# Performance work log

Measured on AMD Instinct MI355X. Metric: run time of the kernel, lower is better.

Reference implementation:

```python
import jax, jax.numpy as jnp
import numpy as np

B, C2, H, W = 4, 1024, 64, 64  # features have 2*input_dim channels
CH = C2 // 2                   # 512 = input_dim
HID = CH // 4                  # 128 = hidden_channels


def setup_inputs() -> dict:
    key = jax.random.key(0)
    ks = jax.random.split(key, 6)
    left = jax.random.normal(ks[0], (B, C2, H, W), dtype=jnp.float32)
    right = jax.random.normal(ks[1], (B, C2, H, W), dtype=jnp.float32)
    # 1x1 conv params (weight [out,in], bias [out]) for query/reference projections
    Wq = jax.random.normal(ks[2], (HID, CH), dtype=jnp.float32) * 0.02
    bq = jax.random.normal(ks[3], (HID,), dtype=jnp.float32) * 0.02
    Wk = jax.random.normal(ks[4], (HID, CH), dtype=jnp.float32) * 0.02
    bk = jax.random.normal(ks[5], (HID,), dtype=jnp.float32) * 0.02
    return {"left_features": left, "right_features": right, "Wq": Wq, "bq": bq, "Wk": Wk, "bk": bk}


def _co_attention(qf, rf, Wq, bq, Wk, bk):
    # 1x1 convs == per-pixel channel matmuls
    Q = jnp.einsum('bchw,oc->bohw', qf, Wq) + bq[None, :, None, None]   # [B,HID,H,W]
    K = jnp.einsum('bchw,oc->bohw', rf, Wk) + bk[None, :, None, None]   # [B,HID,H,W]
    b, c, h, w = Q.shape
    Kf = K.reshape(b, c, h * w)                                          # [B,HID,P]
    V = rf.reshape(rf.shape[0], rf.shape[1], h * w)                      # [B,CH,P]
    # attention_map: einsum('bcij,bckl->bijkl') then flatten (kl) == contract channels
    attn = jnp.einsum('bcij,bcp->bijp', Q, Kf)                           # [B,H,W,P]
    attn = jax.nn.softmax(attn, axis=3)
    return jnp.einsum('bijp,bcp->bcij', attn, V)                         # [B,CH,H,W]


def _homo(qf, rf):
    weights = jax.nn.softmax(qf - rf, axis=1)  # softmax over channels
    return rf * weights


def _get_both_differences(q, r, Wq, bq, Wk, bk):
    c = q.shape[1] // 2
    q_orig, q_trans = q[:, :c], q[:, c:]
    r_orig = r[:, :c]
    cross = _co_attention(q_orig, r_orig, Wq, bq, Wk, bk)
    reduce = _homo(q_orig, q_trans)
    return jnp.concatenate([q_orig, cross + reduce], axis=1)


def reference(left_features, right_features, Wq, bq, Wk, bk):
    left_out = _get_both_differences(left_features, right_features, Wq, bq, Wk, bk)
    right_out = _get_both_differences(right_features, left_features, Wq, bq, Wk, bk)
    return (left_out, right_out)
```

## Files before the change

kernel.cpp:

```cpp
#include <hip/hip_runtime.h>
#include <hip/hip_bf16.h>

#define NB 4
#define LOG2E 1.4426950408889634f

typedef unsigned short u16;
typedef __attribute__((ext_vector_type(8))) short bf16x8;
typedef __attribute__((ext_vector_type(4))) float f32x4;

static __device__ __forceinline__ float bf2f(u16 u) {
    union { float f; unsigned v; } x; x.v = ((unsigned)u) << 16; return x.f;
}
static __device__ __forceinline__ u16 f2bf(float f) {
    unsigned v = __builtin_bit_cast(unsigned, f);
    return (u16)((v + 0x7FFFu + ((v >> 16) & 1u)) >> 16);
}
static __device__ __forceinline__ void gload_lds16(const u16* g, u16* l) {
    __builtin_amdgcn_global_load_lds(
        (const __attribute__((address_space(1))) unsigned*)(const void*)g,
        (__attribute__((address_space(3))) unsigned*)(void*)l, 16, 0, 0);
}

__global__ void k_wcvt(const float* __restrict__ Wq, const float* __restrict__ Wk,
                       u16* __restrict__ Wbq, u16* __restrict__ Wbk) {
    int i = blockIdx.x * 1024 + threadIdx.x;
    Wbq[i] = f2bf(Wq[i]);
    Wbk[i] = f2bf(Wk[i]);
}

__global__ __launch_bounds__(256) void k_cvtf(
        const float* __restrict__ L, const float* __restrict__ R,
        u16* __restrict__ Lb, u16* __restrict__ Rb,
        u16* __restrict__ web, float* __restrict__ sumsH, float* __restrict__ out) {
    __shared__ float pred[4][1024];
    int idx = blockIdx.x;
    int sb = idx & 7, pseg = (idx >> 3) & 3, cpart = idx >> 5;
    int side = sb & 1, b = sb >> 1;
    int osb = side * 4 + b;
    const float* src = (side ? R : L) + (size_t)b * 1024 * 4096;
    u16* lbbase = (side ? Rb : Lb) + (size_t)b * 512 * 4096;
    int tid = threadIdx.x, wv = tid >> 6, lane = tid & 63;
    int p0 = pseg * 1024;
    int cA = cpart * 8 + wv * 2;
#pragma unroll
    for (int s = 0; s < 4; s++) {
        int p = p0 + s * 256 + lane * 4;
        float4 sm = {0.f, 0.f, 0.f, 0.f};
#pragma unroll
        for (int cc = 0; cc < 2; cc++) {
            int c = cA + cc;
            float4 a = *reinterpret_cast<const float4*>(src + (size_t)c * 4096 + p);
            float4 t = *reinterpret_cast<const float4*>(src + (size_t)(512 + c) * 4096 + p);
            ushort4 ub;
            ub.x = f2bf(a.x); ub.y = f2bf(a.y); ub.z = f2bf(a.z); ub.w = f2bf(a.w);
            *reinterpret_cast<ushort4*>(lbbase + (size_t)c * 4096 + p) = ub;
            *reinterpret_cast<float4*>(out + ((size_t)osb * 1024 + c) * 4096 + p) = a;
            float4 e;
            e.x = exp2f((a.x - t.x) * LOG2E);
            e.y = exp2f((a.y - t.y) * LOG2E);
            e.z = exp2f((a.z - t.z) * LOG2E);
            e.w = exp2f((a.w - t.w) * LOG2E);
            sm.x += e.x; sm.y += e.y; sm.z += e.z; sm.w += e.w;
            ushort4 wb_;
            wb_.x = f2bf(t.x * e.x); wb_.y = f2bf(t.y * e.y);
            wb_.z = f2bf(t.z * e.z); wb_.w = f2bf(t.w * e.w);
            *reinterpret_cast<ushort4*>(web + ((size_t)osb * 512 + c) * 4096 + p) = wb_;
        }
        *reinterpret_cast<float4*>(&pred[wv][s * 256 + lane * 4]) = sm;
    }
    __syncthreads();
    {
        float4 t0 = *reinterpret_cast<const float4*>(&pred[0][tid * 4]);
        float4 t1 = *reinterpret_cast<const float4*>(&pred[1][tid * 4]);
        float4 t2 = *reinterpret_cast<const float4*>(&pred[2][tid * 4]);
        float4 t3 = *reinterpret_cast<const float4*>(&pred[3][tid * 4]);
        float4 tot;
        tot.x = (t0.x + t1.x) + (t2.x + t3.x);
        tot.y = (t0.y + t1.y) + (t2.y + t3.y);
        tot.z = (t0.z + t1.z) + (t2.z + t3.z);
        tot.w = (t0.w + t1.w) + (t2.w + t3.w);
        *reinterpret_cast<float4*>(
            sumsH + ((size_t)cpart * 8 + osb) * 4096 + p0 + tid * 4) = tot;
    }
}

__global__ __launch_bounds__(256) void k_hsum(const float* __restrict__ sumsH,
                                              float* __restrict__ hinv) {
    int i = blockIdx.x * 256 + threadIdx.x;
    float4 tot = {0.f, 0.f, 0.f, 0.f};
    for (int cp = 0; cp < 64; cp++) {
        float4 v = *reinterpret_cast<const float4*>(sumsH + (size_t)cp * 8 * 4096 + (size_t)i * 4);
        tot.x += v.x; tot.y += v.y; tot.z += v.z; tot.w += v.w;
    }
    float4 r = {1.0f / tot.x, 1.0f / tot.y, 1.0f / tot.z, 1.0f / tot.w};
    *reinterpret_cast<float4*>(hinv + (size_t)i * 4) = r;
}

__global__ void k_cvt(const float* __restrict__ L, const float* __restrict__ R,
                      u16* __restrict__ Lb, u16* __restrict__ Rb, float* __restrict__ out) {
    int i = blockIdx.x * 256 + threadIdx.x;
    int pq = i & 1023;
    int c = (i >> 10) & 511;
    int b = (i >> 19) & 3;
    int side = i >> 21;
    const float* src = (side ? R : L) + ((long)(b * 1024 + c) << 12) + (pq << 2);
    float4 v = *reinterpret_cast<const float4*>(src);
    ushort4 u;
    u.x = f2bf(v.x); u.y = f2bf(v.y); u.z = f2bf(v.z); u.w = f2bf(v.w);
    *reinterpret_cast<ushort4*>((side ? Rb : Lb) + ((long)(b * 512 + c) << 12) + (pq << 2)) = u;
    *reinterpret_cast<float4*>(out + ((long)(side * 4 + b) * 1024 + c) * 4096 + (pq << 2)) = v;
}

__global__ __launch_bounds__(256) void k_proj(
        const u16* __restrict__ Lb, const u16* __restrict__ Rb,
        const u16* __restrict__ Wbq, const u16* __restrict__ Wbk,
        const float* __restrict__ bq, const float* __restrict__ bk,
        u16* __restrict__ QL, u16* __restrict__ KL,
        u16* __restrict__ QR, u16* __restrict__ KR) {
    __shared__ u16 XT[2][64 * 40];
    int pj = blockIdx.x & 15, pt = blockIdx.x >> 4;
    int ty = pj >> 2, b = pj & 3;
    const u16* src; const u16* Wb; const float* bias; u16* dst;
    if (ty == 0)      { src = Lb; Wb = Wbq; bias = bq; dst = QL; }
    else if (ty == 1) { src = Rb; Wb = Wbk; bias = bk; dst = KL; }
    else if (ty == 2) { src = Rb; Wb = Wbq; bias = bq; dst = QR; }
    else              { src = Lb; Wb = Wbk; bias = bk; dst = KR; }
    const u16* X = src + (long)b * 512 * 4096 + pt * 64;
    int tid = threadIdx.x;
    int wv = __builtin_amdgcn_readfirstlane(tid >> 6);
    int lane = tid & 63, g = lane >> 4, li = lane & 15;

    f32x4 acc[8];
#pragma unroll
    for (int ob = 0; ob < 8; ob++)
#pragma unroll
        for (int r = 0; r < 4; r++) acc[ob][r] = bias[ob * 16 + g * 4 + r];

    int c_r = tid >> 3, j = tid & 7;
    bf16x8 gx = *reinterpret_cast<const bf16x8*>(X + (long)c_r * 4096 + j * 8);
#pragma unroll
    for (int k = 0; k < 8; k++) XT[0][(j * 8 + k) * 40 + c_r] = (u16)gx[k];
    __syncthreads();

    for (int cc = 0; cc < 16; cc++) {
        int buf = cc & 1;
        bf16x8 gn;
        if (cc < 15)
            gn = *reinterpret_cast<const bf16x8*>(X + (long)(cc * 32 + 32 + c_r) * 4096 + j * 8);
        bf16x8 xb = *reinterpret_cast<const bf16x8*>(&XT[buf][(wv * 16 + li) * 40 + g * 8]);
#pragma unroll
        for (int ob = 0; ob < 8; ob++) {
            bf16x8 aw = *reinterpret_cast<const bf16x8*>(Wb + (long)(ob * 16 + li) * 512 + cc * 32 + g * 8);
            acc[ob] = __builtin_amdgcn_mfma_f32_16x16x32_bf16(aw, xb, acc[ob], 0, 0, 0);
        }
        if (cc < 15) {
#pragma unroll
            for (int k = 0; k < 8; k++) XT[buf ^ 1][(j * 8 + k) * 40 + c_r] = (u16)gn[k];
        }
        __syncthreads();
    }
    u16* d = dst + ((long)b * 4096 + pt * 64 + wv * 16 + li) * 128;
#pragma unroll
    for (int ob = 0; ob < 8; ob++) {
        uint2 w;
        w.x = (unsigned)f2bf(acc[ob][0]) | ((unsigned)f2bf(acc[ob][1]) << 16);
        w.y = (unsigned)f2bf(acc[ob][2]) | ((unsigned)f2bf(acc[ob][3]) << 16);
        *reinterpret_cast<uint2*>(d + ob * 16 + g * 4) = w;
    }
}

__global__ __launch_bounds__(512, 8) void k_qk(
        const u16* __restrict__ QL, const u16* __restrict__ KL,
        const u16* __restrict__ QR, const u16* __restrict__ KR,
        u16* __restrict__ P, float* __restrict__ sums,
        int bd0, int nbdLog2) {
    __shared__ u16 Kl[2][8192];
    __shared__ u16 Ps[4096];
    int blk = (int)blockIdx.x;
    int bdl = blk & ((1 << nbdLog2) - 1);
    int rest = blk >> nbdLog2;
    int ph0 = rest & 3;
    int qtile = rest >> 2;
    int bd = bd0 + bdl, dir = bd & 1, b = bd >> 1;
    const u16* Qt = (dir ? QR : QL) + (size_t)b * 4096 * 128;
    const u16* Kt = (dir ? KR : KL) + (size_t)b * 4096 * 128;
    u16* Pbd = P + ((size_t)bdl << 24);
    int q0 = qtile * 64;
    int tid = threadIdx.x;
    int wv = __builtin_amdgcn_readfirstlane(tid >> 6);
    int lane = tid & 63, g = lane >> 4, li = lane & 15;
    int qt = wv >> 1, phw = wv & 1;

#define STAGE_K(BUF, PT)                                                                   \
    {                                                                                      \
        _Pragma("unroll") for (int r0 = 0; r0 < 2; r0++) {                                 \
            int o = r0 * 8192 + tid * 16;                                                  \
            int row = o >> 8, w = o & 255;                                                 \
            int sw = (w ^ ((row & 7) << 4)) >> 1;                                          \
            gload_lds16(Kt + (((size_t)((PT) * 64 + row)) << 7) + sw,                      \
                        &Kl[BUF][r0 * 4096 + wv * 512]);                                   \
        }                                                                                  \
    }

    bf16x8 qf[4];
#pragma unroll
    for (int hc = 0; hc < 4; hc++)
        qf[hc] = *reinterpret_cast<const bf16x8*>(
            Qt + (size_t)(q0 + qt * 16 + li) * 128 + hc * 32 + g * 8);
    float psum = 0.f;
    STAGE_K(0, ph0 * 16)

    for (int tt = 0; tt < 16; tt++) {
        int pt = ph0 * 16 + tt;
        if (tt == 0) asm volatile("s_waitcnt vmcnt(0) lgkmcnt(0)\n\ts_barrier" ::: "memory");
        else         asm volatile("s_waitcnt vmcnt(1) lgkmcnt(0)\n\ts_barrier" ::: "memory");
        if (tt < 15) STAGE_K((tt + 1) & 1, pt + 1)
        int buf = tt & 1;
        f32x4 sv[2];
        sv[0] = (f32x4){0.f, 0.f, 0.f, 0.f};
        sv[1] = (f32x4){0.f, 0.f, 0.f, 0.f};
        __builtin_amdgcn_s_setprio(1);
#pragma unroll
        for (int ps = 0; ps < 2; ps++) {
            int row = phw * 32 + ps * 16 + li;
            unsigned rb = (unsigned)row * 256;
            unsigned sz = (unsigned)((row & 7) << 4);
#pragma unroll
            for (int hc = 0; hc < 4; hc++) {
                bf16x8 kf = *reinterpret_cast<const bf16x8*>(
                    (char*)Kl[buf] + rb + (((unsigned)(hc * 64 + g * 16)) ^ sz));
                sv[ps] = __builtin_amdgcn_mfma_f32_16x16x32_bf16(kf, qf[hc], sv[ps], 0, 0, 0);
            }
        }
        __builtin_amdgcn_s_setprio(0);
        int qrow = qt * 16 + li;
        unsigned qsz = (unsigned)((qrow & 7) << 4);
#pragma unroll
        for (int ps = 0; ps < 2; ps++) {
            float e0 = exp2f(sv[ps][0] * LOG2E);
            float e1 = exp2f(sv[ps][1] * LOG2E);
            float e2 = exp2f(sv[ps][2] * LOG2E);
            float e3 = exp2f(sv[ps][3] * LOG2E);
            psum += (e0 + e1) + (e2 + e3);
            uint2 pk;
            pk.x = (unsigned)f2bf(e0) | ((unsigned)f2bf(e1) << 16);
            pk.y = (unsigned)f2bf(e2) | ((unsigned)f2bf(e3) << 16);
            unsigned off = (unsigned)qrow * 128 +
                           (((unsigned)(phw * 64 + ps * 32 + g * 8)) ^ qsz);
            *reinterpret_cast<uint2*>((char*)Ps + off) = pk;
        }
        asm volatile("s_waitcnt lgkmcnt(0)\n\ts_barrier" ::: "memory");
        {
            uint4 d = *reinterpret_cast<const uint4*>((char*)Ps + tid * 16);
            *reinterpret_cast<uint4*>(
                Pbd + ((size_t)(qtile * 64 + pt) << 12) + tid * 8) = d;
        }
    }
    __syncthreads();
    float (*sred)[2][16] = (float(*)[2][16])(void*)Ps;
    psum += __shfl_xor(psum, 16);
    psum += __shfl_xor(psum, 32);
    if (lane < 16) sred[qt][phw][li] = psum;
    __syncthreads();
    if (phw == 0 && lane < 16) {
        float s = sred[qt][0][li] + sred[qt][1][li];
        sums[((size_t)ph0 * 8 + bd) * 4096 + q0 + qt * 16 + li] = s;
    }
#undef STAGE_K
}

template<int FUSEH>
__global__ __launch_bounds__(256, 2) void k_pvC(
        const u16* __restrict__ Lb, const u16* __restrict__ Rb,
        const u16* __restrict__ P, const float* __restrict__ sums,
        const u16* __restrict__ web, const float* __restrict__ hinvArr,
        float* __restrict__ out, int bd0, int bdMask, int bdShift) {
    __shared__ u16 Tl[2][2][8192];
    int bdl, idx;
    if (bdMask == 3) {
        int xcd = (int)blockIdx.x & 7;
        bdl = xcd >> 1;
        idx = (((int)blockIdx.x >> 3) << 1) | (xcd & 1);
    } else {
        bdl = (int)blockIdx.x & bdMask;
        idx = (int)blockIdx.x >> bdShift;
    }
    int mtile = idx & 3;
    int ntile = idx >> 2;
    int bd = bd0 + bdl, dir = bd & 1, b = bd >> 1;
    int osb = dir * 4 + b;
    const u16* V = (dir ? Lb : Rb) + (size_t)b * 512 * 4096;
    const u16* Pbd = P + ((size_t)bdl << 24);
    int q0 = ntile * 128, c0 = mtile * 128, qt0 = ntile * 2;
    int tid = threadIdx.x;
    int wv = __builtin_amdgcn_readfirstlane(tid >> 6);
    int lane = tid & 63, g = lane >> 4, li = lane & 15;
    int wr = wv >> 1, wc = wv & 1;

#define STAGE_PV(BUF, T)                                                                   \
    {                                                                                      \
        _Pragma("unroll") for (int r0 = 0; r0 < 4; r0++) {                                 \
            int o = r0 * 4096 + tid * 16;                                                  \
            int row = o >> 7, w = o & 127;                                                 \
            int sw = (w ^ ((row & 7) << 4)) >> 1;                                          \
            gload_lds16(V + (((size_t)(c0 + row)) << 12) + (T) * 64 + sw,                  \
                        &Tl[BUF][0][r0 * 2048 + wv * 512]);                                \
            gload_lds16(Pbd + (((size_t)((qt0 + (r0 >> 1)) * 64 + (T))) << 12) +           \
                            (r0 & 1) * 2048 + tid * 8,                                     \
                        &Tl[BUF][1][r0 * 2048 + wv * 512]);                                \
        }                                                                                  \
    }

    f32x4 acc[4][4];
#pragma unroll
    for (int i = 0; i < 4; i++)
#pragma unroll
        for (int j = 0; j < 4; j++) acc[i][j] = (f32x4){0.f, 0.f, 0.f, 0.f};

    STAGE_PV(0, 0)

    for (int t = 0; t < 64; t++) {
        asm volatile("s_waitcnt vmcnt(0) lgkmcnt(0)\n\ts_barrier" ::: "memory");
        if (t < 63) STAGE_PV((t + 1) & 1, t + 1)
        int buf = t & 1;
        bf16x8 af[4][2], bf[4][2];
#pragma unroll
        for (int mi = 0; mi < 4; mi++) {
            int row = wr * 64 + mi * 16 + li;
            unsigned rb = (unsigned)row * 128, sz = (unsigned)((row & 7) << 4);
#pragma unroll
            for (int kk = 0; kk < 2; kk++)
                af[mi][kk] = *reinterpret_cast<const bf16x8*>(
                    (char*)Tl[buf][0] + rb + (((unsigned)(kk * 64 + g * 16)) ^ sz));
        }
#pragma unroll
        for (int ni = 0; ni < 4; ni++) {
            int row = wc * 64 + ni * 16 + li;
            unsigned rb = (unsigned)row * 128, sz = (unsigned)((row & 7) << 4);
#pragma unroll
            for (int kk = 0; kk < 2; kk++)
                bf[ni][kk] = *reinterpret_cast<const bf16x8*>(
                    (char*)Tl[buf][1] + rb + (((unsigned)(kk * 64 + g * 16)) ^ sz));
        }
        __builtin_amdgcn_s_setprio(1);
#pragma unroll
        for (int kk = 0; kk < 2; kk++)
#pragma unroll
            for (int mi = 0; mi < 4; mi++)
#pragma unroll
                for (int ni = 0; ni < 4; ni++)
                    acc[mi][ni] = __builtin_amdgcn_mfma_f32_16x16x32_bf16(
                        af[mi][kk], bf[ni][kk], acc[mi][ni], 0, 0, 0);
        __builtin_amdgcn_s_setprio(0);
    }

    float* obase = out + ((size_t)osb * 1024 + 512) * 4096;
    const u16* wb = web + (size_t)osb * 512 * 4096;
#pragma unroll
    for (int ni = 0; ni < 4; ni++) {
        int q = q0 + wc * 64 + ni * 16 + li;
        float s = sums[(size_t)bd * 4096 + q] +
                  sums[((size_t)8 + bd) * 4096 + q] +
                  sums[((size_t)16 + bd) * 4096 + q] +
                  sums[((size_t)24 + bd) * 4096 + q];
        float linv = 1.0f / s;
        float hinv = 0.f;
        if (FUSEH) hinv = hinvArr[(size_t)osb * 4096 + q];
#pragma unroll
        for (int mi = 0; mi < 4; mi++) {
            int c = c0 + wr * 64 + mi * 16 + g * 4;
#pragma unroll
            for (int r = 0; r < 4; r++) {
                float v = acc[mi][ni][r] * linv;
                if (FUSEH) v += bf2f(wb[(size_t)(c + r) * 4096 + q]) * hinv;
                obase[(size_t)(c + r) * 4096 + q] = v;
            }
        }
    }
#undef STAGE_PV
}

__global__ __launch_bounds__(256) void k_homo(const float* __restrict__ L,
                                              const float* __restrict__ R,
                                              float* __restrict__ out) {
    __shared__ float4 red[16][16];
    int sb = blockIdx.x & 7, pblk = blockIdx.x >> 3;
    int side = sb & 1, b = sb >> 1;
    const float* src = (side ? R : L) + (long)b * 1024 * 4096;
    float* o = out + (long)(side * 4 + b) * 1024 * 4096;
    int p4 = threadIdx.x & 15, cg = threadIdx.x >> 4;
    int p = pblk * 64 + p4 * 4;
    const float* qo = src + p;
    const float* qt = src + (long)512 * 4096 + p;
    float4 sm = {0.f, 0.f, 0.f, 0.f};
    for (int c = cg * 32; c < cg * 32 + 32; c++) {
        float4 a = *reinterpret_cast<const float4*>(qo + (long)c * 4096);
        float4 t = *reinterpret_cast<const float4*>(qt + (long)c * 4096);
        sm.x += exp2f((a.x - t.x) * LOG2E);
        sm.y += exp2f((a.y - t.y) * LOG2E);
        sm.z += exp2f((a.z - t.z) * LOG2E);
        sm.w += exp2f((a.w - t.w) * LOG2E);
    }
    red[cg][p4] = sm;
    __syncthreads();
    float4 tot = {0.f, 0.f, 0.f, 0.f};
#pragma unroll
    for (int gR = 0; gR < 16; gR++) {
        float4 v = red[gR][p4];
        tot.x += v.x; tot.y += v.y; tot.z += v.z; tot.w += v.w;
    }
    float4 rinv = {1.0f / tot.x, 1.0f / tot.y, 1.0f / tot.z, 1.0f / tot.w};
    for (int c = cg * 32; c < cg * 32 + 32; c++) {
        float4 a = *reinterpret_cast<const float4*>(qo + (long)c * 4096);
        float4 t = *reinterpret_cast<const float4*>(qt + (long)c * 4096);
        float4* op = reinterpret_cast<float4*>(o + (long)(512 + c) * 4096 + p);
        float4 cur = *op;
        cur.x += t.x * exp2f((a.x - t.x) * LOG2E) * rinv.x;
        cur.y += t.y * exp2f((a.y - t.y) * LOG2E) * rinv.y;
        cur.z += t.z * exp2f((a.z - t.z) * LOG2E) * rinv.z;
        cur.w += t.w * exp2f((a.w - t.w) * LOG2E) * rinv.w;
        *op = cur;
    }
}

extern "C" void kernel_launch(void* const* d_in, const int* in_sizes, int n_in,
                              void* d_out, int out_size, void* d_ws, size_t ws_size,
                              hipStream_t stream) {
    const float* L  = (const float*)d_in[0];
    const float* R  = (const float*)d_in[1];
    const float* Wq = (const float*)d_in[2];
    const float* bq = (const float*)d_in[3];
    const float* Wk = (const float*)d_in[4];
    const float* bk = (const float*)d_in[5];
    float* out = (float*)d_out;
    char* ws = (char*)d_ws;

    size_t off = 0;
    u16* Wbq = (u16*)(ws + off); off += (size_t)128 * 512 * 2;
    u16* Wbk = (u16*)(ws + off); off += (size_t)128 * 512 * 2;
    u16* QL = (u16*)(ws + off); off += (size_t)NB * 4096 * 128 * 2;
    u16* KL = (u16*)(ws + off); off += (size_t)NB * 4096 * 128 * 2;
    u16* QR = (u16*)(ws + off); off += (size_t)NB * 4096 * 128 * 2;
    u16* KR = (u16*)(ws + off); off += (size_t)NB * 4096 * 128 * 2;
    u16* Lb = (u16*)(ws + off); off += (size_t)NB * 512 * 4096 * 2;
    u16* Rb = (u16*)(ws + off); off += (size_t)NB * 512 * 4096 * 2;
    float* sums = (float*)(ws + off); off += (size_t)4 * 8 * 4096 * 4;
    float* hinv = (float*)(ws + off); off += (size_t)8 * 4096 * 4;
    size_t off_nofuse = off;
    float* sumsH = (float*)(ws + off); off += (size_t)64 * 8 * 4096 * 4;
    u16* web = (u16*)(ws + off); off += (size_t)8 * 512 * 4096 * 2;
    off = (off + 255) & ~(size_t)255;
    size_t pchunk4 = (size_t)4 * 4096 * 4096 * 2;

    k_wcvt <<<64, 1024, 0, stream>>>(Wq, Wk, Wbq, Wbk);

    if (ws_size >= off + pchunk4) {
        u16* Pb = (u16*)(ws + off);
        k_cvtf <<<2048, 256, 0, stream>>>(L, R, Lb, Rb, web, sumsH, out);
        k_hsum <<<32,   256, 0, stream>>>(sumsH, hinv);
        k_proj <<<1024, 256, 0, stream>>>(Lb, Rb, Wbq, Wbk, bq, bk, QL, KL, QR, KR);
        for (int c = 0; c < 2; c++) {
            k_qk     <<<1024, 512, 0, stream>>>(QL, KL, QR, KR, Pb, sums, c * 4, 2);
            k_pvC<1> <<<512,  256, 0, stream>>>(Lb, Rb, Pb, sums, web, hinv, out, c * 4, 3, 2);
        }
    } else {
        size_t poff = (off_nofuse + 255) & ~(size_t)255;
        u16* Pb = (u16*)(ws + poff);
        k_cvt  <<<16384, 256, 0, stream>>>(L, R, Lb, Rb, out);
        k_proj <<<1024,  256, 0, stream>>>(Lb, Rb, Wbq, Wbk, bq, bk, QL, KL, QR, KR);
        for (int c = 0; c < 8; c++) {
            k_qk     <<<256, 512, 0, stream>>>(QL, KL, QR, KR, Pb, sums, c, 0);
            k_pvC<0> <<<128, 256, 0, stream>>>(Lb, Rb, Pb, sums, web, hinv, out, c, 0, 0);
        }
        k_homo <<<512, 256, 0, stream>>>(L, R, out);
    }
}
```

Baseline: 381.6 us.

## Add 256x256-tile PV kernel and single-pass full-P path when workspace allows

After: 430.4 us. +12.8%, slower.

```diff
diff --git a/kernel.cpp b/kernel.cpp
--- a/kernel.cpp
+++ b/kernel.cpp
@@ -270,6 +270,121 @@
 }
 
 template<int FUSEH>
+__global__ __launch_bounds__(512, 1) void k_pv256(
+        const u16* __restrict__ Lb, const u16* __restrict__ Rb,
+        const u16* __restrict__ P, const float* __restrict__ sums,
+        const u16* __restrict__ web, const float* __restrict__ hinvArr,
+        float* __restrict__ out) {
+    __shared__ u16 Va[2][16384];
+    __shared__ u16 Pa[2][16384];
+    int bd = (int)blockIdx.x & 7;
+    int idx = (int)blockIdx.x >> 3;
+    int mt = idx & 1, nt = idx >> 1;
+    int dir = bd & 1, b = bd >> 1, osb = dir * 4 + b;
+    const u16* V = (dir ? Lb : Rb) + (size_t)b * 512 * 4096;
+    const u16* Pbd = P + ((size_t)bd << 24);
+    int c0 = mt * 256, q0 = nt * 256;
+    int tid = threadIdx.x;
+    int wv = __builtin_amdgcn_readfirstlane(tid >> 6);
+    int lane = tid & 63, g = lane >> 4, li = lane & 15;
+    int wr = wv >> 2, wc = wv & 3;
+
+    int vsw = (((tid & 7) * 16) ^ (((tid >> 3) & 7) << 4)) >> 1;
+    const u16* vbase = V + (size_t)(c0 + (tid >> 3)) * 4096 + vsw;
+    const u16* pbase = Pbd + (size_t)tid * 8;
+    int ntq = nt * 256;
+
+#define STG_V(OTH, H, K1)                                                              \
+    gload_lds16(vbase + (size_t)((H) * 128) * 4096 + (K1) * 64,                        \
+                &Va[OTH][(H) * 8192 + wv * 512]);                                      \
+    gload_lds16(vbase + (size_t)((H) * 128 + 64) * 4096 + (K1) * 64,                   \
+                &Va[OTH][(H) * 8192 + 4096 + wv * 512]);
+#define STG_P(OTH, H, K1)                                                              \
+    gload_lds16(pbase + (size_t)(ntq + (H) * 128 + (K1)) * 4096,                       \
+                &Pa[OTH][(H) * 8192 + wv * 512]);                                      \
+    gload_lds16(pbase + (size_t)(ntq + (H) * 128 + 64 + (K1)) * 4096,                  \
+                &Pa[OTH][(H) * 8192 + 4096 + wv * 512]);
+
+#define RD_AF(MB, KK)                                                                  \
+    _Pragma("unroll") for (int m_ = 0; m_ < 4; m_++) {                                 \
+        int row = wr * 128 + ((MB) + m_) * 16 + li;                                    \
+        af[m_] = *reinterpret_cast<const bf16x8*>((char*)Va[bufv] + row * 128 +        \
+                 (((unsigned)((KK) * 64 + g * 16)) ^ ((row & 7) << 4)));               \
+    }
+#define RD_BF(KK)                                                                      \
+    _Pragma("unroll") for (int n_ = 0; n_ < 4; n_++) {                                 \
+        int row = wc * 64 + n_ * 16 + li;                                              \
+        bf[n_] = *reinterpret_cast<const bf16x8*>((char*)Pa[bufv] + row * 128 +        \
+                 (((unsigned)((KK) * 64 + g * 16)) ^ ((row & 7) << 4)));               \
+    }
+#define MM(MB)                                                                         \
+    __builtin_amdgcn_s_setprio(1);                                                     \
+    _Pragma("unroll") for (int m_ = 0; m_ < 4; m_++)                                   \
+        _Pragma("unroll") for (int n_ = 0; n_ < 4; n_++)                               \
+            acc[(MB) + m_][n_] = __builtin_amdgcn_mfma_f32_16x16x32_bf16(              \
+                af[m_], bf[n_], acc[(MB) + m_][n_], 0, 0, 0);                          \
+    __builtin_amdgcn_s_setprio(0);
+
+    f32x4 acc[8][4];
+#pragma unroll
+    for (int i = 0; i < 8; i++)
+#pragma unroll
+        for (int j = 0; j < 4; j++) acc[i][j] = (f32x4){0.f, 0.f, 0.f, 0.f};
+
+    STG_V(0, 0, 0) STG_V(0, 1, 0) STG_P(0, 0, 0) STG_P(0, 1, 0)
+
+    for (int k = 0; k < 64; ++k) {
+        int bufv = k & 1, oth = bufv ^ 1;
+        bf16x8 af[4], bf[4];
+        if (k < 63) {
+            STG_V(oth, 0, k + 1)
+            asm volatile("s_waitcnt vmcnt(2)" ::: "memory");
+        } else {
+            asm volatile("s_waitcnt vmcnt(0)" ::: "memory");
+        }
+        asm volatile("s_barrier" ::: "memory");
+        RD_AF(0, 0) RD_BF(0) MM(0)
+        if (k < 63) { STG_P(oth, 0, k + 1) }
+        RD_AF(4, 0) MM(4)
+        if (k < 63) { STG_V(oth, 1, k + 1) }
+        RD_AF(0, 1) RD_BF(1) MM(0)
+        if (k < 63) { STG_P(oth, 1, k + 1) }
+        RD_AF(4, 1) MM(4)
+        asm volatile("s_waitcnt lgkmcnt(0)" ::: "memory");
+        asm volatile("s_barrier" ::: "memory");
+    }
+
+    float* obase = out + ((size_t)osb * 1024 + 512) * 4096;
+    const u16* wb = web + (size_t)osb * 512 * 4096;
+#pragma unroll
+    for (int ni = 0; ni < 4; ni++) {
+        int q = q0 + wc * 64 + ni * 16 + li;
+        float s = sums[(size_t)bd * 4096 + q] +
+                  sums[((size_t)8 + bd) * 4096 + q] +
+                  sums[((size_t)16 + bd) * 4096 + q] +
+                  sums[((size_t)24 + bd) * 4096 + q];
+        float linv = 1.0f / s;
+        float hinv = 0.f;
+        if (FUSEH) hinv = hinvArr[(size_t)osb * 4096 + q];
+#pragma unroll
+        for (int mi = 0; mi < 8; mi++) {
+            int c = c0 + wr * 128 + mi * 16 + g * 4;
+#pragma unroll
+            for (int r = 0; r < 4; r++) {
+                float v = acc[mi][ni][r] * linv;
+                if (FUSEH) v += bf2f(wb[(size_t)(c + r) * 4096 + q]) * hinv;
+                obase[(size_t)(c + r) * 4096 + q] = v;
+            }
+        }
+    }
+#undef STG_V
+#undef STG_P
+#undef RD_AF
+#undef RD_BF
+#undef MM
+}
+
+template<int FUSEH>
 __global__ __launch_bounds__(256, 2) void k_pvC(
         const u16* __restrict__ Lb, const u16* __restrict__ Rb,
         const u16* __restrict__ P, const float* __restrict__ sums,
@@ -451,10 +566,18 @@
     u16* web = (u16*)(ws + off); off += (size_t)8 * 512 * 4096 * 2;
     off = (off + 255) & ~(size_t)255;
     size_t pchunk4 = (size_t)4 * 4096 * 4096 * 2;
+    size_t pfull   = (size_t)8 * 4096 * 4096 * 2;
 
     k_wcvt <<<64, 1024, 0, stream>>>(Wq, Wk, Wbq, Wbk);
 
-    if (ws_size >= off + pchunk4) {
+    if (ws_size >= off + pfull) {
+        u16* Pb = (u16*)(ws + off);
+        k_cvtf     <<<2048, 256, 0, stream>>>(L, R, Lb, Rb, web, sumsH, out);
+        k_hsum     <<<32,   256, 0, stream>>>(sumsH, hinv);
+        k_proj     <<<1024, 256, 0, stream>>>(Lb, Rb, Wbq, Wbk, bq, bk, QL, KL, QR, KR);
+        k_qk       <<<2048, 512, 0, stream>>>(QL, KL, QR, KR, Pb, sums, 0, 3);
+        k_pv256<1> <<<256,  512, 0, stream>>>(Lb, Rb, Pb, sums, web, hinv, out);
+    } else if (ws_size >= off + pchunk4) {
         u16* Pb = (u16*)(ws + off);
         k_cvtf <<<2048, 256, 0, stream>>>(L, R, Lb, Rb, web, sumsH, out);
         k_hsum <<<32,   256, 0, stream>>>(sumsH, hinv);
```

## Process all eight batch-directions in one QK and new larger-tile PV kernel

Applied to the files above, without the earlier changes.

Result: slower. 407.6 us (+6.8%).

```diff
diff --git a/kernel.cpp b/kernel.cpp
--- a/kernel.cpp
+++ b/kernel.cpp
@@ -270,6 +270,134 @@
 }
 
 template<int FUSEH>
+__global__ __launch_bounds__(256, 2) void k_pvD(
+        const u16* __restrict__ Lb, const u16* __restrict__ Rb,
+        const u16* __restrict__ P, const float* __restrict__ sums,
+        const u16* __restrict__ web, const float* __restrict__ hinvArr,
+        float* __restrict__ out) {
+    __shared__ u16 Va[2][8192];
+    __shared__ u16 Pl[2][4096];
+    int bd = (int)blockIdx.x & 7;
+    int idx = (int)blockIdx.x >> 3;
+    int mtile = idx & 1, ntile = idx >> 1;
+    int dir = bd & 1, b = bd >> 1, osb = dir * 4 + b;
+    const u16* V = (dir ? Lb : Rb) + (size_t)b * 512 * 4096;
+    const u16* Pbd = P + ((size_t)bd << 24);
+    int q0 = ntile * 128, c0 = mtile * 256;
+    int tid = threadIdx.x;
+    int wv = __builtin_amdgcn_readfirstlane(tid >> 6);
+    int lane = tid & 63, g = lane >> 4, li = lane & 15;
+    int wr = wv >> 1, wc = wv & 1;
+
+    const u16 *vsrc0, *vsrc1, *vsrc2, *vsrc3;
+    {
+        int o, row, wd;
+        o = tid * 16;          row = o >> 6; wd = (o & 63) ^ (((row >> 1) & 3) << 4);
+        vsrc0 = V + (size_t)(c0 + row) * 4096 + (wd >> 1);
+        o = 4096 + tid * 16;   row = o >> 6; wd = (o & 63) ^ (((row >> 1) & 3) << 4);
+        vsrc1 = V + (size_t)(c0 + row) * 4096 + (wd >> 1);
+        o = 8192 + tid * 16;   row = o >> 6; wd = (o & 63) ^ (((row >> 1) & 3) << 4);
+        vsrc2 = V + (size_t)(c0 + row) * 4096 + (wd >> 1);
+        o = 12288 + tid * 16;  row = o >> 6; wd = (o & 63) ^ (((row >> 1) & 3) << 4);
+        vsrc3 = V + (size_t)(c0 + row) * 4096 + (wd >> 1);
+    }
+    const u16 *pb0, *pb1;
+    int pOff0a, pOff0b, pOff1a, pOff1b;
+    {
+        int o, row, wd, q, qr;
+        o = tid * 16; row = o >> 6; wd = (o & 63) ^ (((row >> 1) & 3) << 4);
+        q = q0 + row; qr = q & 63;
+        pb0 = Pbd + (((size_t)((q >> 6) * 64)) << 12) + qr * 64;
+        pOff0a = ((0  + wd) ^ ((qr & 7) << 4)) >> 1;
+        pOff0b = ((64 + wd) ^ ((qr & 7) << 4)) >> 1;
+        o = 4096 + tid * 16; row = o >> 6; wd = (o & 63) ^ (((row >> 1) & 3) << 4);
+        q = q0 + row; qr = q & 63;
+        pb1 = Pbd + (((size_t)((q >> 6) * 64)) << 12) + qr * 64;
+        pOff1a = ((0  + wd) ^ ((qr & 7) << 4)) >> 1;
+        pOff1b = ((64 + wd) ^ ((qr & 7) << 4)) >> 1;
+    }
+
+#define STAGE_D(BUF, T)                                                                    \
+    {                                                                                      \
+        int pt_ = (T) >> 1, pc_ = (T) & 1;                                                 \
+        gload_lds16(vsrc0 + (T) * 32, &Va[BUF][wv * 512]);                                 \
+        gload_lds16(vsrc1 + (T) * 32, &Va[BUF][2048 + wv * 512]);                          \
+        gload_lds16(vsrc2 + (T) * 32, &Va[BUF][4096 + wv * 512]);                          \
+        gload_lds16(vsrc3 + (T) * 32, &Va[BUF][6144 + wv * 512]);                          \
+        gload_lds16(pb0 + ((size_t)pt_ << 12) + (pc_ ? pOff0b : pOff0a),                   \
+                    &Pl[BUF][wv * 512]);                                                   \
+        gload_lds16(pb1 + ((size_t)pt_ << 12) + (pc_ ? pOff1b : pOff1a),                   \
+                    &Pl[BUF][2048 + wv * 512]);                                            \
+    }
+
+    unsigned aoff[8], boff[4];
+#pragma unroll
+    for (int mi = 0; mi < 8; mi++) {
+        int row = wr * 128 + mi * 16 + li;
+        aoff[mi] = (unsigned)row * 64 + (((unsigned)(g * 16)) ^ (((row >> 1) & 3) << 4));
+    }
+#pragma unroll
+    for (int ni = 0; ni < 4; ni++) {
+        int row = wc * 64 + ni * 16 + li;
+        boff[ni] = (unsigned)row * 64 + (((unsigned)(g * 16)) ^ (((row >> 1) & 3) << 4));
+    }
+
+    f32x4 acc[8][4];
+#pragma unroll
+    for (int i = 0; i < 8; i++)
+#pragma unroll
+        for (int j = 0; j < 4; j++) acc[i][j] = (f32x4){0.f, 0.f, 0.f, 0.f};
+
+    STAGE_D(0, 0)
+
+    for (int t = 0; t < 128; t++) {
+        asm volatile("s_waitcnt vmcnt(0) lgkmcnt(0)\n\ts_barrier" ::: "memory");
+        if (t < 127) STAGE_D((t + 1) & 1, t + 1)
+        int buf = t & 1;
+        bf16x8 af[8], bf[4];
+#pragma unroll
+        for (int mi = 0; mi < 8; mi++)
+            af[mi] = *reinterpret_cast<const bf16x8*>((char*)Va[buf] + aoff[mi]);
+#pragma unroll
+        for (int ni = 0; ni < 4; ni++)
+            bf[ni] = *reinterpret_cast<const bf16x8*>((char*)Pl[buf] + boff[ni]);
+        __builtin_amdgcn_s_setprio(1);
+#pragma unroll
+        for (int mi = 0; mi < 8; mi++)
+#pragma unroll
+            for (int ni = 0; ni < 4; ni++)
+                acc[mi][ni] = __builtin_amdgcn_mfma_f32_16x16x32_bf16(
+                    af[mi], bf[ni], acc[mi][ni], 0, 0, 0);
+        __builtin_amdgcn_s_setprio(0);
+    }
+
+    float* obase = out + ((size_t)osb * 1024 + 512) * 4096;
+    const u16* wb = web + (size_t)osb * 512 * 4096;
+#pragma unroll
+    for (int ni = 0; ni < 4; ni++) {
+        int q = q0 + wc * 64 + ni * 16 + li;
+        float s = sums[(size_t)bd * 4096 + q] +
+                  sums[((size_t)8 + bd) * 4096 + q] +
+                  sums[((size_t)16 + bd) * 4096 + q] +
+                  sums[((size_t)24 + bd) * 4096 + q];
+        float linv = 1.0f / s;
+        float hinv = 0.f;
+        if (FUSEH) hinv = hinvArr[(size_t)osb * 4096 + q];
+#pragma unroll
+        for (int mi = 0; mi < 8; mi++) {
+            int c = c0 + wr * 128 + mi * 16 + g * 4;
+#pragma unroll
+            for (int r = 0; r < 4; r++) {
+                float v = acc[mi][ni][r] * linv;
+                if (FUSEH) v += bf2f(wb[(size_t)(c + r) * 4096 + q]) * hinv;
+                obase[(size_t)(c + r) * 4096 + q] = v;
+            }
+        }
+    }
+#undef STAGE_D
+}
+
+template<int FUSEH>
 __global__ __launch_bounds__(256, 2) void k_pvC(
         const u16* __restrict__ Lb, const u16* __restrict__ Rb,
         const u16* __restrict__ P, const float* __restrict__ sums,
@@ -451,10 +579,18 @@
     u16* web = (u16*)(ws + off); off += (size_t)8 * 512 * 4096 * 2;
     off = (off + 255) & ~(size_t)255;
     size_t pchunk4 = (size_t)4 * 4096 * 4096 * 2;
+    size_t pfull   = (size_t)8 * 4096 * 4096 * 2;
 
     k_wcvt <<<64, 1024, 0, stream>>>(Wq, Wk, Wbq, Wbk);
 
-    if (ws_size >= off + pchunk4) {
+    if (ws_size >= off + pfull) {
+        u16* Pb = (u16*)(ws + off);
+        k_cvtf   <<<2048, 256, 0, stream>>>(L, R, Lb, Rb, web, sumsH, out);
+        k_hsum   <<<32,   256, 0, stream>>>(sumsH, hinv);
+        k_proj   <<<1024, 256, 0, stream>>>(Lb, Rb, Wbq, Wbk, bq, bk, QL, KL, QR, KR);
+        k_qk     <<<2048, 512, 0, stream>>>(QL, KL, QR, KR, Pb, sums, 0, 3);
+        k_pvD<1> <<<512,  256, 0, stream>>>(Lb, Rb, Pb, sums, web, hinv, out);
+    } else if (ws_size >= off + pchunk4) {
         u16* Pb = (u16*)(ws + off);
         k_cvtf <<<2048, 256, 0, stream>>>(L, R, Lb, Rb, web, sumsH, out);
         k_hsum <<<32,   256, 0, stream>>>(sumsH, hinv);
```

## Process all batch-directions in one QK/PV launch when workspace allows; nontemporal stores

Applied to the files above, without the earlier changes.

After: 392.0 us. +2.7%, slower.

```diff
diff --git a/kernel.cpp b/kernel.cpp
--- a/kernel.cpp
+++ b/kernel.cpp
@@ -7,6 +7,7 @@
 typedef unsigned short u16;
 typedef __attribute__((ext_vector_type(8))) short bf16x8;
 typedef __attribute__((ext_vector_type(4))) float f32x4;
+typedef __attribute__((ext_vector_type(4))) unsigned short u16x4;
 
 static __device__ __forceinline__ float bf2f(u16 u) {
     union { float f; unsigned v; } x; x.v = ((unsigned)u) << 16; return x.f;
@@ -19,6 +20,12 @@
     __builtin_amdgcn_global_load_lds(
         (const __attribute__((address_space(1))) unsigned*)(const void*)g,
         (__attribute__((address_space(3))) unsigned*)(void*)l, 16, 0, 0);
+}
+static __device__ __forceinline__ void nts_f4(float* p, float4 v) {
+    __builtin_nontemporal_store(__builtin_bit_cast(f32x4, v), (f32x4*)p);
+}
+static __device__ __forceinline__ void nts_u4(u16* p, ushort4 v) {
+    __builtin_nontemporal_store(__builtin_bit_cast(u16x4, v), (u16x4*)p);
 }
 
 __global__ void k_wcvt(const float* __restrict__ Wq, const float* __restrict__ Wk,
@@ -45,26 +52,31 @@
 #pragma unroll
     for (int s = 0; s < 4; s++) {
         int p = p0 + s * 256 + lane * 4;
-        float4 sm = {0.f, 0.f, 0.f, 0.f};
-#pragma unroll
-        for (int cc = 0; cc < 2; cc++) {
-            int c = cA + cc;
-            float4 a = *reinterpret_cast<const float4*>(src + (size_t)c * 4096 + p);
-            float4 t = *reinterpret_cast<const float4*>(src + (size_t)(512 + c) * 4096 + p);
-            ushort4 ub;
-            ub.x = f2bf(a.x); ub.y = f2bf(a.y); ub.z = f2bf(a.z); ub.w = f2bf(a.w);
-            *reinterpret_cast<ushort4*>(lbbase + (size_t)c * 4096 + p) = ub;
-            *reinterpret_cast<float4*>(out + ((size_t)osb * 1024 + c) * 4096 + p) = a;
-            float4 e;
-            e.x = exp2f((a.x - t.x) * LOG2E);
-            e.y = exp2f((a.y - t.y) * LOG2E);
-            e.z = exp2f((a.z - t.z) * LOG2E);
-            e.w = exp2f((a.w - t.w) * LOG2E);
-            sm.x += e.x; sm.y += e.y; sm.z += e.z; sm.w += e.w;
-            ushort4 wb_;
-            wb_.x = f2bf(t.x * e.x); wb_.y = f2bf(t.y * e.y);
-            wb_.z = f2bf(t.z * e.z); wb_.w = f2bf(t.w * e.w);
-            *reinterpret_cast<ushort4*>(web + ((size_t)osb * 512 + c) * 4096 + p) = wb_;
+        float4 a0 = *reinterpret_cast<const float4*>(src + (size_t)cA * 4096 + p);
+        float4 t0 = *reinterpret_cast<const float4*>(src + (size_t)(512 + cA) * 4096 + p);
+        float4 a1 = *reinterpret_cast<const float4*>(src + (size_t)(cA + 1) * 4096 + p);
+        float4 t1 = *reinterpret_cast<const float4*>(src + (size_t)(512 + cA + 1) * 4096 + p);
+        float4 sm;
+        {
+            float4 e0, e1;
+            e0.x = exp2f((a0.x - t0.x) * LOG2E); e0.y = exp2f((a0.y - t0.y) * LOG2E);
+            e0.z = exp2f((a0.z - t0.z) * LOG2E); e0.w = exp2f((a0.w - t0.w) * LOG2E);
+            e1.x = exp2f((a1.x - t1.x) * LOG2E); e1.y = exp2f((a1.y - t1.y) * LOG2E);
+            e1.z = exp2f((a1.z - t1.z) * LOG2E); e1.w = exp2f((a1.w - t1.w) * LOG2E);
+            sm.x = e0.x + e1.x; sm.y = e0.y + e1.y; sm.z = e0.z + e1.z; sm.w = e0.w + e1.w;
+            ushort4 ub0, ub1, wb0, wb1;
+            ub0.x = f2bf(a0.x); ub0.y = f2bf(a0.y); ub0.z = f2bf(a0.z); ub0.w = f2bf(a0.w);
+            ub1.x = f2bf(a1.x); ub1.y = f2bf(a1.y); ub1.z = f2bf(a1.z); ub1.w = f2bf(a1.w);
+            wb0.x = f2bf(t0.x * e0.x); wb0.y = f2bf(t0.y * e0.y);
+            wb0.z = f2bf(t0.z * e0.z); wb0.w = f2bf(t0.w * e0.w);
+            wb1.x = f2bf(t1.x * e1.x); wb1.y = f2bf(t1.y * e1.y);
+            wb1.z = f2bf(t1.z * e1.z); wb1.w = f2bf(t1.w * e1.w);
+            *reinterpret_cast<ushort4*>(lbbase + (size_t)cA * 4096 + p) = ub0;
+            *reinterpret_cast<ushort4*>(lbbase + (size_t)(cA + 1) * 4096 + p) = ub1;
+            nts_f4(out + ((size_t)osb * 1024 + cA) * 4096 + p, a0);
+            nts_f4(out + ((size_t)osb * 1024 + cA + 1) * 4096 + p, a1);
+            nts_u4(web + ((size_t)osb * 512 + cA) * 4096 + p, wb0);
+            nts_u4(web + ((size_t)osb * 512 + cA + 1) * 4096 + p, wb1);
         }
         *reinterpret_cast<float4*>(&pred[wv][s * 256 + lane * 4]) = sm;
     }
@@ -277,7 +289,10 @@
         float* __restrict__ out, int bd0, int bdMask, int bdShift) {
     __shared__ u16 Tl[2][2][8192];
     int bdl, idx;
-    if (bdMask == 3) {
+    if (bdMask == 7) {
+        bdl = (int)blockIdx.x & 7;
+        idx = (int)blockIdx.x >> 3;
+    } else if (bdMask == 3) {
         int xcd = (int)blockIdx.x & 7;
         bdl = xcd >> 1;
         idx = (((int)blockIdx.x >> 3) << 1) | (xcd & 1);
@@ -451,10 +466,18 @@
     u16* web = (u16*)(ws + off); off += (size_t)8 * 512 * 4096 * 2;
     off = (off + 255) & ~(size_t)255;
     size_t pchunk4 = (size_t)4 * 4096 * 4096 * 2;
+    size_t pfull   = (size_t)8 * 4096 * 4096 * 2;
 
     k_wcvt <<<64, 1024, 0, stream>>>(Wq, Wk, Wbq, Wbk);
 
-    if (ws_size >= off + pchunk4) {
+    if (ws_size >= off + pfull) {
+        u16* Pb = (u16*)(ws + off);
+        k_cvtf   <<<2048, 256, 0, stream>>>(L, R, Lb, Rb, web, sumsH, out);
+        k_hsum   <<<32,   256, 0, stream>>>(sumsH, hinv);
+        k_proj   <<<1024, 256, 0, stream>>>(Lb, Rb, Wbq, Wbk, bq, bk, QL, KL, QR, KR);
+        k_qk     <<<2048, 512, 0, stream>>>(QL, KL, QR, KR, Pb, sums, 0, 3);
+        k_pvC<1> <<<1024, 256, 0, stream>>>(Lb, Rb, Pb, sums, web, hinv, out, 0, 7, 3);
+    } else if (ws_size >= off + pchunk4) {
         u16* Pb = (u16*)(ws + off);
         k_cvtf <<<2048, 256, 0, stream>>>(L, R, Lb, Rb, web, sumsH, out);
         k_hsum <<<32,   256, 0, stream>>>(sumsH, hinv);
```
